# Optimization experiments

Measured on AMD Instinct MI355X. Metric: run time of the kernel, lower is better.

Reference implementation:

```python
import jax, jax.numpy as jnp
import numpy as np

HIDDEN = 2048
IN = 2
OUT = 2
T = 1024


def setup_inputs() -> dict:
    key = jax.random.key(0)
    ks = jax.random.split(key, 8)
    s_ih = 1.0 / np.sqrt(HIDDEN)
    return {
        "features": jax.random.normal(ks[0], (1, HIDDEN), dtype=jnp.float32),
        "point_cloud": jax.random.normal(ks[1], (1, T, IN), dtype=jnp.float32),
        "W_ih": jax.random.uniform(ks[2], (4 * HIDDEN, IN), jnp.float32, -s_ih, s_ih),
        "W_hh": jax.random.uniform(ks[3], (4 * HIDDEN, HIDDEN), jnp.float32, -s_ih, s_ih),
        "b_ih": jax.random.uniform(ks[4], (4 * HIDDEN,), jnp.float32, -s_ih, s_ih),
        "b_hh": jax.random.uniform(ks[5], (4 * HIDDEN,), jnp.float32, -s_ih, s_ih),
        "W_fc": jax.random.uniform(ks[6], (OUT, HIDDEN), jnp.float32, -s_ih, s_ih),
        "b_fc": jax.random.uniform(ks[7], (OUT,), jnp.float32, -s_ih, s_ih),
        "max_seq_len": T,
    }


def reference(features, point_cloud, W_ih, W_hh, b_ih, b_hh, W_fc, b_fc, max_seq_len):
    # Training branch of DecoderRNN.forward: teacher-forced LSTMCell decode.
    H = features.shape[1]
    c0 = jnp.zeros_like(features)  # [B, H]

    def step(carry, x_t):
        h, c = carry
        gates = x_t @ W_ih.T + b_ih + h @ W_hh.T + b_hh  # [B, 4H]
        i, f, g, o = jnp.split(gates, 4, axis=-1)  # PyTorch LSTMCell gate order
        c_new = jax.nn.sigmoid(f) * c + jax.nn.sigmoid(i) * jnp.tanh(g)
        h_new = jax.nn.sigmoid(o) * jnp.tanh(c_new)
        out = h_new @ W_fc.T + b_fc  # [B, OUT]
        return (h_new, c_new), out

    xs = jnp.swapaxes(point_cloud, 0, 1)  # [T, B, IN]
    _, outs = jax.lax.scan(step, (features, c0), xs)  # outs: [T, B, OUT]
    # original returns outputs[:, 1:, :] which drops the initial zeros row
    return jnp.swapaxes(outs, 0, 1)  # [B, T, OUT]
```

## Files before the change

kernel.cpp:

```cpp
#include <hip/hip_runtime.h>
#include <math.h>
#include <stdint.h>

#define HIDDEN 2048
#define TSTEPS 1024
#define NWG 256
#define TPB 512
#define UPW 8
#define CPT 16
#define CHUNK_QW 6
#define STEP_QW (NWG * CHUNK_QW)
#define GO_STRIDE 32
#define FLAG_STRIDE 32

__device__ __forceinline__ float sigmoidf_(float x) { return 1.0f / (1.0f + __expf(-x)); }

__global__ __launch_bounds__(TPB, 2)
void lstm_v8(const float* __restrict__ features,
             const float* __restrict__ pc,
             const float* __restrict__ W_ih,
             const float* __restrict__ W_hh,
             const float* __restrict__ b_ih,
             const float* __restrict__ b_hh,
             const float* __restrict__ W_fc,
             const float* __restrict__ b_fc,
             float* __restrict__ out,
             int*      __restrict__ go,
             uint64_t* __restrict__ hh)
{
    const int b    = blockIdx.x;
    const int t    = threadIdx.x;
    const int lane = t & 63;
    const int wave = t >> 6;
    const int g    = t & 3;
    const int cc   = t >> 2;
    const int col0 = cc * CPT;

    __builtin_amdgcn_fence(__ATOMIC_ACQUIRE, "agent");

    __shared__ float pc_sh[2 * TSTEPS];
    __shared__ float red[8 * 32];
    __shared__ float outred[16];

    {
        const float4* p4 = reinterpret_cast<const float4*>(pc);
        reinterpret_cast<float4*>(pc_sh)[t] = p4[t];
    }

    float w[UPW][CPT];
    {
        const int baserow = g * HIDDEN + b * UPW;
        #pragma unroll
        for (int ji = 0; ji < UPW; ++ji) {
            const float4* src = reinterpret_cast<const float4*>(
                W_hh + (size_t)(baserow + ji) * HIDDEN + col0);
            float4 a0 = src[0], a1 = src[1], a2 = src[2], a3 = src[3];
            w[ji][0]  = a0.x; w[ji][1]  = a0.y; w[ji][2]  = a0.z; w[ji][3]  = a0.w;
            w[ji][4]  = a1.x; w[ji][5]  = a1.y; w[ji][6]  = a1.z; w[ji][7]  = a1.w;
            w[ji][8]  = a2.x; w[ji][9]  = a2.y; w[ji][10] = a2.z; w[ji][11] = a2.w;
            w[ji][12] = a3.x; w[ji][13] = a3.y; w[ji][14] = a3.z; w[ji][15] = a3.w;
        }
    }

    float bias_r = 0.0f, wi0_r = 0.0f, wi1_r = 0.0f, creg = 0.0f;
    if (wave == 0) {
        const int l   = lane & 31;
        const int row = (l >> 3) * HIDDEN + b * UPW + (l & 7);
        bias_r = b_ih[row] + b_hh[row];
        wi0_r  = W_ih[row * 2 + 0];
        wi1_r  = W_ih[row * 2 + 1];
    }
    __syncthreads();

    for (int s = 0; s < TSTEPS; ++s) {
        const int rot = (s >= 1) && (b == ((s - 1) & 255));

        float hr[CPT];
        if (s == 0) {
            #pragma unroll
            for (int k = 0; k < CPT; k += 4) {
                float4 hv = *reinterpret_cast<const float4*>(features + col0 + k);
                hr[k] = hv.x; hr[k + 1] = hv.y; hr[k + 2] = hv.z; hr[k + 3] = hv.w;
            }
        } else {
            const uint64_t* qp = hh + (size_t)s * STEP_QW + (size_t)(cc * 2) * CHUNK_QW;
            const uint32_t tagexp = (uint32_t)s;
            #pragma unroll
            for (int c2 = 0; c2 < 2; ++c2) {
                uint64_t q[CHUNK_QW];
                const ulonglong2* qp2 = reinterpret_cast<const ulonglong2*>(qp + c2 * CHUNK_QW);
                ulonglong2 u0 = qp2[0], u1 = qp2[1], u2 = qp2[2];
                q[0] = u0.x; q[1] = u0.y; q[2] = u1.x;
                q[3] = u1.y; q[4] = u2.x; q[5] = u2.y;
                #pragma unroll
                for (int j = 0; j < CHUNK_QW; ++j) {
                    if ((uint32_t)(q[j] >> 48) != tagexp) {
                        do {
                            q[j] = __hip_atomic_load(qp + c2 * CHUNK_QW + j,
                                                     __ATOMIC_RELAXED, __HIP_MEMORY_SCOPE_AGENT);
                        } while ((uint32_t)(q[j] >> 48) != tagexp);
                    }
                }
                uint32_t H[3 * CHUNK_QW];
                #pragma unroll
                for (int j = 0; j < CHUNK_QW; ++j) {
                    H[3 * j + 0] = (uint32_t)(q[j] >> 32) & 0xFFFFu;
                    H[3 * j + 1] = (uint32_t)(q[j] >> 16) & 0xFFFFu;
                    H[3 * j + 2] = (uint32_t)(q[j] >>  0) & 0xFFFFu;
                }
                #pragma unroll
                for (int i = 0; i < 8; ++i) {
                    hr[c2 * 8 + i] = __uint_as_float(H[2 * i] | (H[2 * i + 1] << 16));
                }
            }
        }

        float acc[UPW];
        #pragma unroll
        for (int ji = 0; ji < UPW; ++ji) acc[ji] = 0.0f;
        #pragma unroll
        for (int k = 0; k < CPT; ++k) {
            #pragma unroll
            for (int ji = 0; ji < UPW; ++ji) acc[ji] += w[ji][k] * hr[k];
        }
        #pragma unroll
        for (int m = 4; m < 64; m <<= 1) {
            #pragma unroll
            for (int ji = 0; ji < UPW; ++ji) acc[ji] += __shfl_xor(acc[ji], m);
        }
        if (lane < 4) {
            #pragma unroll
            for (int ji = 0; ji < UPW; ++ji) red[wave * 32 + lane * 8 + ji] = acc[ji];
        }

        if (rot) {
            float po0 = 0.0f, po1 = 0.0f;
            #pragma unroll
            for (int k = 0; k < CPT; ++k) {
                po0 += hr[k] * W_fc[col0 + k];
                po1 += hr[k] * W_fc[HIDDEN + col0 + k];
            }
            #pragma unroll
            for (int m = 1; m < 64; m <<= 1) {
                po0 += __shfl_xor(po0, m);
                po1 += __shfl_xor(po1, m);
            }
            if (lane == 0) { outred[wave * 2 + 0] = po0; outred[wave * 2 + 1] = po1; }
        }
        __syncthreads();

        const size_t pubbase = (size_t)(s + 1) * STEP_QW;

        if (wave == 0) {
            const int l = lane & 31;
            float sum = 0.0f;
            #pragma unroll
            for (int ww = 0; ww < 8; ++ww) sum += red[ww * 32 + l];
            const float x0 = pc_sh[2 * s], x1 = pc_sh[2 * s + 1];
            const float gate = sum + bias_r + wi0_r * x0 + wi1_r * x1;
            const float iv = __shfl(gate, (lane & 7));
            const float fv = __shfl(gate, 8 + (lane & 7));
            const float gv = __shfl(gate, 16 + (lane & 7));
            const float ov = __shfl(gate, 24 + (lane & 7));
            const float cnew = sigmoidf_(fv) * creg + sigmoidf_(iv) * tanhf(gv);
            const float hnew = sigmoidf_(ov) * tanhf(cnew);
            creg = cnew;
            const uint32_t hb = __float_as_uint(hnew);

            uint64_t v = ((uint64_t)(uint32_t)(s + 1)) << 48;
            #pragma unroll
            for (int i = 0; i < 3; ++i) {
                const int m  = 3 * lane + i;
                const int mc = (m < 16) ? m : 15;
                const uint32_t bits = __shfl(hb, mc >> 1);
                const uint32_t half = (mc & 1) ? (bits >> 16) : (bits & 0xFFFFu);
                if (m < 16) v |= (uint64_t)half << (32 - 16 * i);
            }
            if (lane < CHUNK_QW) {
                __hip_atomic_store(hh + pubbase + (size_t)b * CHUNK_QW + lane,
                                   v, __ATOMIC_RELAXED, __HIP_MEMORY_SCOPE_AGENT);
            }
        }

        if (b == NWG - 1 && wave == 7) {
            const uint32_t tagexp = (uint32_t)(s + 1);
            const int l4 = lane * 4;
            const uint64_t* p0 = hh + pubbase + (size_t)(l4 + 0) * CHUNK_QW + 5;
            const uint64_t* p1 = hh + pubbase + (size_t)(l4 + 1) * CHUNK_QW + 5;
            const uint64_t* p2 = hh + pubbase + (size_t)(l4 + 2) * CHUNK_QW + 5;
            const uint64_t* p3 = hh + pubbase + (size_t)(l4 + 3) * CHUNK_QW + 5;
            for (;;) {
                const uint64_t q0 = __hip_atomic_load(p0, __ATOMIC_RELAXED, __HIP_MEMORY_SCOPE_AGENT);
                const uint64_t q1 = __hip_atomic_load(p1, __ATOMIC_RELAXED, __HIP_MEMORY_SCOPE_AGENT);
                const uint64_t q2 = __hip_atomic_load(p2, __ATOMIC_RELAXED, __HIP_MEMORY_SCOPE_AGENT);
                const uint64_t q3 = __hip_atomic_load(p3, __ATOMIC_RELAXED, __HIP_MEMORY_SCOPE_AGENT);
                const bool ok = ((uint32_t)(q0 >> 48) == tagexp) &
                                ((uint32_t)(q1 >> 48) == tagexp) &
                                ((uint32_t)(q2 >> 48) == tagexp) &
                                ((uint32_t)(q3 >> 48) == tagexp);
                if (__all(ok)) break;
            }
            __hip_atomic_store(go + (size_t)lane * GO_STRIDE, s + 1,
                               __ATOMIC_RELAXED, __HIP_MEMORY_SCOPE_AGENT);
        }

        if (rot && t == 64) {
            float o0 = 0.0f, o1 = 0.0f;
            #pragma unroll
            for (int ww = 0; ww < 8; ++ww) { o0 += outred[ww * 2]; o1 += outred[ww * 2 + 1]; }
            out[(s - 1) * 2 + 0] = 0.25f * o0 + b_fc[0];
            out[(s - 1) * 2 + 1] = 0.25f * o1 + b_fc[1];
        }

        if (t == 0 && b != NWG - 1) {
            const int* gop = go + (size_t)(b >> 2) * GO_STRIDE;
            while (__hip_atomic_load(gop, __ATOMIC_RELAXED,
                                     __HIP_MEMORY_SCOPE_AGENT) < s + 1) {}
        }
        __syncthreads();
    }

    if (b == NWG - 1) {
        const uint64_t* qp = hh + (size_t)TSTEPS * STEP_QW + (size_t)(cc * 2) * CHUNK_QW;
        const uint32_t tagexp = (uint32_t)TSTEPS;
        float hv[CPT];
        #pragma unroll
        for (int c2 = 0; c2 < 2; ++c2) {
            uint64_t q[CHUNK_QW];
            const ulonglong2* qp2 = reinterpret_cast<const ulonglong2*>(qp + c2 * CHUNK_QW);
            ulonglong2 u0 = qp2[0], u1 = qp2[1], u2 = qp2[2];
            q[0] = u0.x; q[1] = u0.y; q[2] = u1.x;
            q[3] = u1.y; q[4] = u2.x; q[5] = u2.y;
            #pragma unroll
            for (int j = 0; j < CHUNK_QW; ++j) {
                if ((uint32_t)(q[j] >> 48) != tagexp) {
                    do {
                        q[j] = __hip_atomic_load(qp + c2 * CHUNK_QW + j,
                                                 __ATOMIC_RELAXED, __HIP_MEMORY_SCOPE_AGENT);
                    } while ((uint32_t)(q[j] >> 48) != tagexp);
                }
            }
            uint32_t H[3 * CHUNK_QW];
            #pragma unroll
            for (int j = 0; j < CHUNK_QW; ++j) {
                H[3 * j + 0] = (uint32_t)(q[j] >> 32) & 0xFFFFu;
                H[3 * j + 1] = (uint32_t)(q[j] >> 16) & 0xFFFFu;
                H[3 * j + 2] = (uint32_t)(q[j] >>  0) & 0xFFFFu;
            }
            #pragma unroll
            for (int i = 0; i < 8; ++i) {
                hv[c2 * 8 + i] = __uint_as_float(H[2 * i] | (H[2 * i + 1] << 16));
            }
        }
        float po0 = 0.0f, po1 = 0.0f;
        #pragma unroll
        for (int k = 0; k < CPT; ++k) {
            po0 += hv[k] * W_fc[col0 + k];
            po1 += hv[k] * W_fc[HIDDEN + col0 + k];
        }
        #pragma unroll
        for (int m = 1; m < 64; m <<= 1) {
            po0 += __shfl_xor(po0, m);
            po1 += __shfl_xor(po1, m);
        }
        if (lane == 0) { outred[wave * 2 + 0] = po0; outred[wave * 2 + 1] = po1; }
        __syncthreads();
        if (t == 0) {
            float o0 = 0.0f, o1 = 0.0f;
            #pragma unroll
            for (int ww = 0; ww < 8; ++ww) { o0 += outred[ww * 2]; o1 += outred[ww * 2 + 1]; }
            out[(TSTEPS - 1) * 2 + 0] = 0.25f * o0 + b_fc[0];
            out[(TSTEPS - 1) * 2 + 1] = 0.25f * o1 + b_fc[1];
        }
    }
}

__global__ __launch_bounds__(TPB, 2)
void lstm_v6(const float* __restrict__ features,
             const float* __restrict__ pc,
             const float* __restrict__ W_ih,
             const float* __restrict__ W_hh,
             const float* __restrict__ b_ih,
             const float* __restrict__ b_hh,
             const float* __restrict__ W_fc,
             const float* __restrict__ b_fc,
             float* __restrict__ out,
             int*   __restrict__ flags,
             int*   __restrict__ go,
             float* __restrict__ hhist)
{
    const int b    = blockIdx.x;
    const int t    = threadIdx.x;
    const int lane = t & 63;
    const int wave = t >> 6;
    __builtin_amdgcn_fence(__ATOMIC_ACQUIRE, "agent");
    const int g    = t & 3;
    const int cc   = t >> 2;
    const int col0 = cc * CPT;
    const bool watcher = (b == NWG - 1) && (wave == 0);

    __shared__ float pc_sh[2 * TSTEPS];
    __shared__ float red[8 * 32];
    __shared__ float outred[16];

    {
        const float4* p4 = reinterpret_cast<const float4*>(pc);
        reinterpret_cast<float4*>(pc_sh)[t] = p4[t];
    }
    float w[UPW][CPT];
    {
        const int baserow = g * HIDDEN + b * UPW;
        #pragma unroll
        for (int ji = 0; ji < UPW; ++ji) {
            const float4* src = reinterpret_cast<const float4*>(
                W_hh + (size_t)(baserow + ji) * HIDDEN + col0);
            float4 a0 = src[0], a1 = src[1], a2 = src[2], a3 = src[3];
            w[ji][0]  = a0.x; w[ji][1]  = a0.y; w[ji][2]  = a0.z; w[ji][3]  = a0.w;
            w[ji][4]  = a1.x; w[ji][5]  = a1.y; w[ji][6]  = a1.z; w[ji][7]  = a1.w;
            w[ji][8]  = a2.x; w[ji][9]  = a2.y; w[ji][10] = a2.z; w[ji][11] = a2.w;
            w[ji][12] = a3.x; w[ji][13] = a3.y; w[ji][14] = a3.z; w[ji][15] = a3.w;
        }
    }
    float bias_r = 0.0f, wi0_r = 0.0f, wi1_r = 0.0f, creg = 0.0f;
    if (wave == 0) {
        const int l   = lane & 31;
        const int row = (l >> 3) * HIDDEN + b * UPW + (l & 7);
        bias_r = b_ih[row] + b_hh[row];
        wi0_r  = W_ih[row * 2 + 0];
        wi1_r  = W_ih[row * 2 + 1];
    }
    __syncthreads();

    for (int s = 0; s < TSTEPS; ++s) {
        const int rot = (s >= 1) && (b == ((s - 1) & 255));
        const float* hsrc = (s == 0) ? features : (hhist + (size_t)s * HIDDEN);
        float hr[CPT];
        #pragma unroll
        for (int k = 0; k < CPT; k += 4) {
            float4 hv = *reinterpret_cast<const float4*>(hsrc + col0 + k);
            hr[k] = hv.x; hr[k + 1] = hv.y; hr[k + 2] = hv.z; hr[k + 3] = hv.w;
        }
        float acc[UPW];
        #pragma unroll
        for (int ji = 0; ji < UPW; ++ji) acc[ji] = 0.0f;
        #pragma unroll
        for (int k = 0; k < CPT; ++k) {
            #pragma unroll
            for (int ji = 0; ji < UPW; ++ji) acc[ji] += w[ji][k] * hr[k];
        }
        #pragma unroll
        for (int m = 4; m < 64; m <<= 1) {
            #pragma unroll
            for (int ji = 0; ji < UPW; ++ji) acc[ji] += __shfl_xor(acc[ji], m);
        }
        if (lane < 4) {
            #pragma unroll
            for (int ji = 0; ji < UPW; ++ji) red[wave * 32 + lane * 8 + ji] = acc[ji];
        }
        if (rot) {
            float po0 = 0.0f, po1 = 0.0f;
            #pragma unroll
            for (int k = 0; k < CPT; ++k) {
                po0 += hr[k] * W_fc[col0 + k];
                po1 += hr[k] * W_fc[HIDDEN + col0 + k];
            }
            #pragma unroll
            for (int m = 1; m < 64; m <<= 1) {
                po0 += __shfl_xor(po0, m);
                po1 += __shfl_xor(po1, m);
            }
            if (lane == 0) { outred[wave * 2 + 0] = po0; outred[wave * 2 + 1] = po1; }
        }
        __syncthreads();

        if (wave == 0) {
            const int l = lane & 31;
            float sum = 0.0f;
            #pragma unroll
            for (int ww = 0; ww < 8; ++ww) sum += red[ww * 32 + l];
            const float x0 = pc_sh[2 * s], x1 = pc_sh[2 * s + 1];
            const float gate = sum + bias_r + wi0_r * x0 + wi1_r * x1;
            const float iv = __shfl(gate, (lane & 7));
            const float fv = __shfl(gate, 8 + (lane & 7));
            const float gv = __shfl(gate, 16 + (lane & 7));
            const float ov = __shfl(gate, 24 + (lane & 7));
            const float cnew = sigmoidf_(fv) * creg + sigmoidf_(iv) * tanhf(gv);
            const float hnew = sigmoidf_(ov) * tanhf(cnew);
            creg = cnew;
            const uint32_t hb = __float_as_uint(hnew);
            const uint32_t lo = __shfl(hb, 2 * (lane & 3));
            const uint32_t hi = __shfl(hb, 2 * (lane & 3) + 1);
            if (lane < 4) {
                const uint64_t qv = (uint64_t)lo | ((uint64_t)hi << 32);
                uint64_t* dst = reinterpret_cast<uint64_t*>(
                    hhist + (size_t)(s + 1) * HIDDEN + b * UPW) + lane;
                __hip_atomic_store(dst, qv, __ATOMIC_RELAXED, __HIP_MEMORY_SCOPE_AGENT);
            }
            asm volatile("s_waitcnt vmcnt(0)" ::: "memory");
            if (lane == 0) {
                __hip_atomic_store(flags + (size_t)b * FLAG_STRIDE, s + 1,
                                   __ATOMIC_RELAXED, __HIP_MEMORY_SCOPE_AGENT);
            }
        }
        if (rot && t == 64) {
            float o0 = 0.0f, o1 = 0.0f;
            #pragma unroll
            for (int ww = 0; ww < 8; ++ww) { o0 += outred[ww * 2]; o1 += outred[ww * 2 + 1]; }
            out[(s - 1) * 2 + 0] = 0.25f * o0 + b_fc[0];
            out[(s - 1) * 2 + 1] = 0.25f * o1 + b_fc[1];
        }
        if (watcher) {
            const int l4 = lane * 4;
            const int* f0p = flags + (size_t)(l4 + 0) * FLAG_STRIDE;
            const int* f1p = flags + (size_t)(l4 + 1) * FLAG_STRIDE;
            const int* f2p = flags + (size_t)(l4 + 2) * FLAG_STRIDE;
            const int* f3p = flags + (size_t)(l4 + 3) * FLAG_STRIDE;
            for (;;) {
                const int f0 = __hip_atomic_load(f0p, __ATOMIC_RELAXED, __HIP_MEMORY_SCOPE_AGENT);
                const int f1 = __hip_atomic_load(f1p, __ATOMIC_RELAXED, __HIP_MEMORY_SCOPE_AGENT);
                const int f2 = __hip_atomic_load(f2p, __ATOMIC_RELAXED, __HIP_MEMORY_SCOPE_AGENT);
                const int f3 = __hip_atomic_load(f3p, __ATOMIC_RELAXED, __HIP_MEMORY_SCOPE_AGENT);
                const bool ok = (f0 >= s + 1) & (f1 >= s + 1) & (f2 >= s + 1) & (f3 >= s + 1);
                if (__all(ok)) break;
            }
            __hip_atomic_store(go + (size_t)lane * GO_STRIDE, s + 1,
                               __ATOMIC_RELAXED, __HIP_MEMORY_SCOPE_AGENT);
        }
        if (t == 0 && b != NWG - 1) {
            const int* gop = go + (size_t)(b >> 2) * GO_STRIDE;
            while (__hip_atomic_load(gop, __ATOMIC_RELAXED,
                                     __HIP_MEMORY_SCOPE_AGENT) < s + 1) {}
        }
        __syncthreads();
    }

    if (b == ((TSTEPS - 1) & 255)) {
        const float* hsrc = hhist + (size_t)TSTEPS * HIDDEN;
        float po0 = 0.0f, po1 = 0.0f;
        #pragma unroll
        for (int k = 0; k < CPT; ++k) {
            const float hv = hsrc[col0 + k];
            po0 += hv * W_fc[col0 + k];
            po1 += hv * W_fc[HIDDEN + col0 + k];
        }
        #pragma unroll
        for (int m = 1; m < 64; m <<= 1) {
            po0 += __shfl_xor(po0, m);
            po1 += __shfl_xor(po1, m);
        }
        if (lane == 0) { outred[wave * 2 + 0] = po0; outred[wave * 2 + 1] = po1; }
        __syncthreads();
        if (t == 0) {
            float o0 = 0.0f, o1 = 0.0f;
            #pragma unroll
            for (int ww = 0; ww < 8; ++ww) { o0 += outred[ww * 2]; o1 += outred[ww * 2 + 1]; }
            out[(TSTEPS - 1) * 2 + 0] = 0.25f * o0 + b_fc[0];
            out[(TSTEPS - 1) * 2 + 1] = 0.25f * o1 + b_fc[1];
        }
    }
}

extern "C" void kernel_launch(void* const* d_in, const int* in_sizes, int n_in,
                              void* d_out, int out_size, void* d_ws, size_t ws_size,
                              hipStream_t stream) {
    const float* features = (const float*)d_in[0];
    const float* pc       = (const float*)d_in[1];
    const float* W_ih     = (const float*)d_in[2];
    const float* W_hh     = (const float*)d_in[3];
    const float* b_ih     = (const float*)d_in[4];
    const float* b_hh     = (const float*)d_in[5];
    const float* W_fc     = (const float*)d_in[6];
    const float* b_fc     = (const float*)d_in[7];
    float* out = (float*)d_out;

    const size_t go_bytes = (size_t)64 * GO_STRIDE * sizeof(int);
    const size_t hh_bytes = (size_t)(TSTEPS + 1) * STEP_QW * sizeof(uint64_t);
    const size_t need_v8  = go_bytes + hh_bytes;

    if (ws_size >= need_v8) {
        int*      go = (int*)d_ws;
        uint64_t* hh = (uint64_t*)((char*)d_ws + go_bytes);
        hipMemsetAsync(d_ws, 0, need_v8, stream);
        hipLaunchKernelGGL(lstm_v8, dim3(NWG), dim3(TPB), 0, stream,
                           features, pc, W_ih, W_hh, b_ih, b_hh, W_fc, b_fc,
                           out, go, hh);
    } else {
        const size_t flags_bytes = (size_t)NWG * FLAG_STRIDE * sizeof(int);
        const size_t hh_off      = flags_bytes + go_bytes;
        int*   flags = (int*)d_ws;
        int*   go    = (int*)((char*)d_ws + flags_bytes);
        float* hhist = (float*)((char*)d_ws + hh_off);
        hipMemsetAsync(d_ws, 0, hh_off, stream);
        hipLaunchKernelGGL(lstm_v6, dim3(NWG), dim3(TPB), 0, stream,
                           features, pc, W_ih, W_hh, b_ih, b_hh, W_fc, b_fc,
                           out, flags, go, hhist);
    }
}
```

Before: 3.705 ms.

## Elect per-XCD relay blocks and poll an XCD-local go flag through L2

Each block reads its XCD id and races for a per-XCD election slot. The winning block on each XCD spins on the step's published hidden-state tags, then writes an XCD-local go flag with a plain store and a global go flag with an agent-scope atomic. Waiting blocks poll the local flag with an sc0 load, which should hit the shared XCD L2 instead of going device-wide, and check the global flag every 16 iterations as a fallback. The intent is to cut the latency of the per-step barrier. The cost is eight pollers scanning all tags instead of one, and the plain-store visibility across L2 is not guaranteed, so correctness relies on the periodic global check.

```diff
diff --git a/kernel.cpp b/kernel.cpp
--- a/kernel.cpp
+++ b/kernel.cpp
@@ -12,11 +12,20 @@
 #define STEP_QW (NWG * CHUNK_QW)
 #define GO_STRIDE 32
 #define FLAG_STRIDE 32
+#define NXCD 8
 
 __device__ __forceinline__ float sigmoidf_(float x) { return 1.0f / (1.0f + __expf(-x)); }
 
+__device__ __forceinline__ int load_go_sc0(const int* p) {
+    int v;
+    asm volatile("global_load_dword %0, %1, off sc0\n\t"
+                 "s_waitcnt vmcnt(0)"
+                 : "=v"(v) : "v"(p) : "memory");
+    return v;
+}
+
 __global__ __launch_bounds__(TPB, 2)
-void lstm_v8(const float* __restrict__ features,
+void lstm_v9(const float* __restrict__ features,
              const float* __restrict__ pc,
              const float* __restrict__ W_ih,
              const float* __restrict__ W_hh,
@@ -25,7 +34,9 @@
              const float* __restrict__ W_fc,
              const float* __restrict__ b_fc,
              float* __restrict__ out,
-             int*      __restrict__ go,
+             int*      __restrict__ elect,
+             int*      __restrict__ go_l,
+             int*      __restrict__ go_glob,
              uint64_t* __restrict__ hh)
 {
     const int b    = blockIdx.x;
@@ -38,9 +49,22 @@
 
     __builtin_amdgcn_fence(__ATOMIC_ACQUIRE, "agent");
 
+    uint32_t xcdreg;
+    asm volatile("s_getreg_b32 %0, hwreg(HW_REG_XCC_ID)" : "=s"(xcdreg));
+    const int myxcd = (int)(xcdreg & (NXCD - 1));
+
     __shared__ float pc_sh[2 * TSTEPS];
     __shared__ float red[8 * 32];
     __shared__ float outred[16];
+    __shared__ int   ls_relay;
+
+    if (t == 0) {
+        int expected = 0;
+        const bool won = __hip_atomic_compare_exchange_strong(
+            elect + (size_t)myxcd * GO_STRIDE, &expected, 1,
+            __ATOMIC_RELAXED, __ATOMIC_RELAXED, __HIP_MEMORY_SCOPE_AGENT);
+        ls_relay = won ? 1 : 0;
+    }
 
     {
         const float4* p4 = reinterpret_cast<const float4*>(pc);
@@ -71,6 +95,7 @@
         wi1_r  = W_ih[row * 2 + 1];
     }
     __syncthreads();
+    const bool isrelay = (ls_relay != 0);
 
     for (int s = 0; s < TSTEPS; ++s) {
         const int rot = (s >= 1) && (b == ((s - 1) & 255));
@@ -182,7 +207,7 @@
             }
         }
 
-        if (b == NWG - 1 && wave == 7) {
+        if (isrelay && wave == 7) {
             const uint32_t tagexp = (uint32_t)(s + 1);
             const int l4 = lane * 4;
             const uint64_t* p0 = hh + pubbase + (size_t)(l4 + 0) * CHUNK_QW + 5;
@@ -200,7 +225,11 @@
                                 ((uint32_t)(q3 >> 48) == tagexp);
                 if (__all(ok)) break;
             }
-            __hip_atomic_store(go + (size_t)lane * GO_STRIDE, s + 1,
+            if (lane == 0) {
+                go_l[(size_t)myxcd * GO_STRIDE] = s + 1;
+                asm volatile("" ::: "memory");
+            }
+            __hip_atomic_store(go_glob + (size_t)lane * GO_STRIDE, s + 1,
                                __ATOMIC_RELAXED, __HIP_MEMORY_SCOPE_AGENT);
         }
 
@@ -212,10 +241,17 @@
             out[(s - 1) * 2 + 1] = 0.25f * o1 + b_fc[1];
         }
 
-        if (t == 0 && b != NWG - 1) {
-            const int* gop = go + (size_t)(b >> 2) * GO_STRIDE;
-            while (__hip_atomic_load(gop, __ATOMIC_RELAXED,
-                                     __HIP_MEMORY_SCOPE_AGENT) < s + 1) {}
+        if (t == 0) {
+            const int* lp = go_l + (size_t)myxcd * GO_STRIDE;
+            const int* gp = go_glob + (size_t)(b >> 2) * GO_STRIDE;
+            int it = 0;
+            for (;;) {
+                if (load_go_sc0(lp) >= s + 1) break;
+                if ((++it & 15) == 0) {
+                    if (__hip_atomic_load(gp, __ATOMIC_RELAXED,
+                                          __HIP_MEMORY_SCOPE_AGENT) >= s + 1) break;
+                }
+            }
         }
         __syncthreads();
     }
@@ -473,24 +509,30 @@
     const float* b_fc     = (const float*)d_in[7];
     float* out = (float*)d_out;
 
-    const size_t go_bytes = (size_t)64 * GO_STRIDE * sizeof(int);
-    const size_t hh_bytes = (size_t)(TSTEPS + 1) * STEP_QW * sizeof(uint64_t);
-    const size_t need_v8  = go_bytes + hh_bytes;
-
-    if (ws_size >= need_v8) {
-        int*      go = (int*)d_ws;
-        uint64_t* hh = (uint64_t*)((char*)d_ws + go_bytes);
-        hipMemsetAsync(d_ws, 0, need_v8, stream);
-        hipLaunchKernelGGL(lstm_v8, dim3(NWG), dim3(TPB), 0, stream,
+    const size_t elect_bytes = (size_t)NXCD * GO_STRIDE * sizeof(int);
+    const size_t gol_bytes   = (size_t)NXCD * GO_STRIDE * sizeof(int);
+    const size_t gog_bytes   = (size_t)64 * GO_STRIDE * sizeof(int);
+    const size_t hh_off      = 16384;
+    const size_t hh_bytes    = (size_t)(TSTEPS + 1) * STEP_QW * sizeof(uint64_t);
+    const size_t need_v9     = hh_off + hh_bytes;
+
+    if (ws_size >= need_v9) {
+        int*      elect = (int*)d_ws;
+        int*      go_l  = (int*)((char*)d_ws + elect_bytes);
+        int*      go_g  = (int*)((char*)d_ws + elect_bytes + gol_bytes);
+        uint64_t* hh    = (uint64_t*)((char*)d_ws + hh_off);
+        hipMemsetAsync(d_ws, 0, need_v9, stream);
+        hipLaunchKernelGGL(lstm_v9, dim3(NWG), dim3(TPB), 0, stream,
                            features, pc, W_ih, W_hh, b_ih, b_hh, W_fc, b_fc,
-                           out, go, hh);
+                           out, elect, go_l, go_g, hh);
     } else {
         const size_t flags_bytes = (size_t)NWG * FLAG_STRIDE * sizeof(int);
-        const size_t hh_off      = flags_bytes + go_bytes;
+        const size_t go_bytes    = (size_t)64 * GO_STRIDE * sizeof(int);
+        const size_t hhf_off     = flags_bytes + go_bytes;
         int*   flags = (int*)d_ws;
         int*   go    = (int*)((char*)d_ws + flags_bytes);
-        float* hhist = (float*)((char*)d_ws + hh_off);
-        hipMemsetAsync(d_ws, 0, hh_off, stream);
+        float* hhist = (float*)((char*)d_ws + hhf_off);
+        hipMemsetAsync(d_ws, 0, hhf_off, stream);
         hipLaunchKernelGGL(lstm_v6, dim3(NWG), dim3(TPB), 0, stream,
                            features, pc, W_ih, W_hh, b_ih, b_hh, W_fc, b_fc,
                            out, flags, go, hhist);
```

Result: slower. 5.138 ms (+38.7%).
